# Optimization experiments

Measured on AMD Instinct MI355X. Metric: run time of the kernel, lower is better.

The kernel has to match this reference:

```python
import jax, jax.numpy as jnp
import numpy as np

N_NODES = 50000
N_EDGES = 800000
IN_DIM, HID_DIM, LAT_DIM = 64, 64, 32


def _glorot(key, fan_in, fan_out):
    s = jnp.sqrt(6.0 / (fan_in + fan_out))
    return jax.random.uniform(key, (fan_in, fan_out), jnp.float32, -s, s)


def setup_inputs() -> dict:
    key = jax.random.key(0)
    ks = jax.random.split(key, 8)
    x = jax.random.normal(ks[0], (N_NODES, IN_DIM), jnp.float32)
    edge_index = jax.random.randint(ks[1], (2, N_EDGES), 0, N_NODES, jnp.int64)
    W1 = _glorot(ks[2], IN_DIM, HID_DIM)
    b1 = jnp.zeros((HID_DIM,), jnp.float32)
    W2 = _glorot(ks[3], HID_DIM, HID_DIM)
    b2 = jnp.zeros((HID_DIM,), jnp.float32)
    W3 = _glorot(ks[4], HID_DIM, LAT_DIM)
    b3 = jnp.zeros((LAT_DIM,), jnp.float32)
    return {"x": x, "edge_index": edge_index, "W1": W1, "b1": b1,
            "W2": W2, "b2": b2, "W3": W3, "b3": b3}


def _self_loop_edges(edge_index, n):
    loop = jnp.arange(n, dtype=edge_index.dtype)
    src = jnp.concatenate([edge_index[0], loop])
    dst = jnp.concatenate([edge_index[1], loop])
    return src, dst


def _gcn_norm(src, dst, n):
    # deg over A + I (unit edge weights), computed on target column (PyG default)
    deg = jax.ops.segment_sum(jnp.ones_like(dst, dtype=jnp.float32), dst, num_segments=n)
    dinv = jnp.where(deg > 0, jax.lax.rsqrt(deg), 0.0)
    return dinv[src] * dinv[dst]  # [E+N]


def _gcn_conv(x, src, dst, norm, W, b, n):
    h = x @ W                         # [N, out] small GEMM first, as in PyG
    msg = h[src] * norm[:, None]      # gather + scale, [E+N, out]
    out = jax.ops.segment_sum(msg, dst, num_segments=n)  # scatter-add
    return out + b


def reference(x, edge_index, W1, b1, W2, b2, W3, b3):
    n = x.shape[0]
    src, dst = _self_loop_edges(edge_index, n)
    norm = _gcn_norm(src, dst, n)
    h = jnp.tanh(_gcn_conv(x, src, dst, norm, W1, b1, n))
    h = jnp.tanh(_gcn_conv(h, src, dst, norm, W2, b2, n))
    z = _gcn_conv(h, src, dst, norm, W3, b3, n)
    return z
```

## Files before the change

### kernel.cpp

```cpp
#include <hip/hip_runtime.h>
#include <hip/hip_fp16.h>
#include <type_traits>


#define IN_DIM 64
#define HID_DIM 64
#define LAT_DIM 32
#define BCAP 5120

typedef __attribute__((ext_vector_type(8))) _Float16 half8;
typedef __attribute__((ext_vector_type(4))) _Float16 half4;


__global__ __launch_bounds__(256) void bin_kernel(const int* __restrict__ src,
                                                  const int* __restrict__ dst,
                                                  int* __restrict__ bucket_cnt,
                                                  unsigned* __restrict__ pairs, int E) {
    __shared__ int bcnt[256];
    __shared__ int bbase[256];
    int tid = threadIdx.x;
    bcnt[tid] = 0;
    __syncthreads();
    int base = blockIdx.x * 4096;
    unsigned pk[16]; int bk[16]; int rk[16];
    #pragma unroll
    for (int i = 0; i < 16; ++i) {
        int e = base + i * 256 + tid;
        bk[i] = -1;
        if (e < E) {
            int s = __builtin_nontemporal_load(src + e);
            int d = __builtin_nontemporal_load(dst + e);
            bk[i] = d >> 8;
            pk[i] = (unsigned)s | ((unsigned)(d & 255) << 16);
            rk[i] = atomicAdd(&bcnt[bk[i]], 1);
        }
    }
    __syncthreads();
    int c = bcnt[tid];
    if (c > 0) bbase[tid] = atomicAdd(&bucket_cnt[tid], c);
    __syncthreads();
    #pragma unroll
    for (int i = 0; i < 16; ++i) {
        if (bk[i] >= 0) {
            int pos = bbase[bk[i]] + rk[i];
            if (pos < BCAP) pairs[(size_t)bk[i] * BCAP + pos] = pk[i];
        }
    }
}

__global__ __launch_bounds__(256) void build_csr_kernel(const unsigned* __restrict__ pairs,
                                                        const int* __restrict__ bucket_cnt,
                                                        int* __restrict__ off,
                                                        float* __restrict__ dinv,
                                                        int* __restrict__ col,
                                                        int N, int NBK) {
    __shared__ int sboff[256];
    __shared__ int h[256];
    __shared__ int scur[256];
    __shared__ int wtot[4];
    int b = blockIdx.x, tid = threadIdx.x;
    int lane = tid & 63, wid = tid >> 6;

    int v = (tid < NBK) ? min(bucket_cnt[tid], BCAP) : 0;
    int sc = v;
    #pragma unroll
    for (int d = 1; d < 64; d <<= 1) {
        int t = __shfl_up(sc, d, 64);
        if (lane >= d) sc += t;
    }
    if (lane == 63) wtot[wid] = sc;
    h[tid] = 0;
    __syncthreads();
    int woff = 0;
    #pragma unroll
    for (int w = 0; w < 4; ++w) if (w < wid) woff += wtot[w];
    sboff[tid] = woff + sc - v;
    __syncthreads();
    int boff_b = sboff[b];

    int c = min(bucket_cnt[b], BCAP);
    const unsigned* pb = pairs + (size_t)b * BCAP;
    for (int i = tid; i < c; i += 256)
        atomicAdd(&h[pb[i] >> 16], 1);
    __syncthreads();

    int hv = h[tid];
    int sc2 = hv;
    #pragma unroll
    for (int d = 1; d < 64; d <<= 1) {
        int t = __shfl_up(sc2, d, 64);
        if (lane >= d) sc2 += t;
    }
    if (lane == 63) wtot[wid] = sc2;
    __syncthreads();
    int woff2 = 0;
    #pragma unroll
    for (int w = 0; w < 4; ++w) if (w < wid) woff2 += wtot[w];
    int incl = woff2 + sc2;
    int node = b * 256 + tid;
    scur[tid] = boff_b + incl - hv;
    if (node < N) {
        off[node + 1] = boff_b + incl;
        dinv[node]    = rsqrtf((float)(hv + 1));
    }
    if (b == 0 && tid == 0) off[0] = 0;
    __syncthreads();

    for (int i = tid; i < c; i += 256) {
        unsigned p = pb[i];
        int pos = atomicAdd(&scur[p >> 16], 1);
        col[pos] = (int)(p & 0xFFFFu);
    }
}


template<int OUT, int RT, typename TIN>
__global__ __launch_bounds__(256) void gemm_tile_kernel(const TIN* __restrict__ X,
                                                        const float* __restrict__ W,
                                                        const float* __restrict__ dinv,
                                                        _Float16* __restrict__ G, int N) {
    constexpr int CG = OUT / 4;
    static_assert(256 / CG * 4 == RT, "RT must match 4*(256/CG)");
    __shared__ float Ws[64 * OUT];
    __shared__ float Xs[RT][64 + 4];
    int tid = threadIdx.x;
    int row0 = blockIdx.x * RT;

    for (int f = 4 * tid; f < 64 * OUT; f += 1024)
        *(float4*)&Ws[f] = *(const float4*)&W[f];

    if constexpr (std::is_same<TIN, float>::value) {
        for (int f = 4 * tid; f < RT * 64; f += 1024) {
            int r = f >> 6, k0 = f & 63, gr = row0 + r;
            float4 v = (gr < N) ? *(const float4*)&X[(size_t)gr * 64 + k0]
                                : make_float4(0.f, 0.f, 0.f, 0.f);
            *(float4*)&Xs[r][k0] = v;
        }
    } else {
        for (int f = 8 * tid; f < RT * 64; f += 2048) {
            int r = f >> 6, k0 = f & 63, gr = row0 + r;
            if (gr < N) {
                half8 v = *(const half8*)&X[(size_t)gr * 64 + k0];
                #pragma unroll
                for (int i = 0; i < 8; ++i) Xs[r][k0 + i] = (float)v[i];
            } else {
                #pragma unroll
                for (int i = 0; i < 8; ++i) Xs[r][k0 + i] = 0.f;
            }
        }
    }
    __syncthreads();

    int cr = tid % CG;
    int rr = tid / CG;
    float acc[4][4] = {};
    #pragma unroll 4
    for (int k = 0; k < 64; ++k) {
        float4 bv = *(float4*)&Ws[k * OUT + 4 * cr];
        float av[4] = {Xs[4 * rr + 0][k], Xs[4 * rr + 1][k],
                       Xs[4 * rr + 2][k], Xs[4 * rr + 3][k]};
        float bb[4] = {bv.x, bv.y, bv.z, bv.w};
        #pragma unroll
        for (int j = 0; j < 4; ++j)
            #pragma unroll
            for (int i = 0; i < 4; ++i)
                acc[j][i] += av[j] * bb[i];
    }

    #pragma unroll
    for (int j = 0; j < 4; ++j) {
        int gr = row0 + 4 * rr + j;
        if (gr < N) {
            float s = dinv[gr];
            half4 o;
            #pragma unroll
            for (int i = 0; i < 4; ++i) o[i] = (_Float16)(acc[j][i] * s);
            *(half4*)&G[(size_t)gr * OUT + 4 * cr] = o;
        }
    }
}


template<int D, bool TANH, typename TOUT>
__global__ __launch_bounds__(256) void agg_kernel(const _Float16* __restrict__ G,
                           const int* __restrict__ off,
                           const int* __restrict__ col, const float* __restrict__ dinv,
                           const float* __restrict__ b, TOUT* __restrict__ H, int N) {
    constexpr int CHUNKS = D / 8;
    constexpr int EPI = 64 / CHUNKS;
    int tid  = threadIdx.x;
    int lane = tid & 63;
    int w    = tid >> 6;
    int node = blockIdx.x * 4 + w;
    if (node >= N) return;
    int grp = lane / CHUNKS;
    int c4  = lane % CHUNKS;
    int p0  = off[node];
    int total = off[node + 1] - p0 + 1;
    float acc[8] = {};
    #pragma unroll 2
    for (int base = 0; base < total; base += EPI) {
        int e = base + grp;
        if (e < total) {
            int s = (e == 0) ? node : col[p0 + e - 1];
            half8 u = *(const half8*)&G[(size_t)s * D + 8 * c4];
            #pragma unroll
            for (int i = 0; i < 8; ++i) acc[i] += (float)u[i];
        }
    }
    #pragma unroll
    for (int m = CHUNKS; m < 64; m <<= 1) {
        #pragma unroll
        for (int i = 0; i < 8; ++i) acc[i] += __shfl_xor(acc[i], m, 64);
    }
    if (grp == 0) {
        float s = dinv[node];
        float o[8];
        #pragma unroll
        for (int i = 0; i < 8; ++i) {
            o[i] = s * acc[i] + b[8 * c4 + i];
            if (TANH) o[i] = tanhf(o[i]);
        }
        if constexpr (std::is_same<TOUT, _Float16>::value) {
            half8 hv;
            #pragma unroll
            for (int i = 0; i < 8; ++i) hv[i] = (_Float16)o[i];
            *(half8*)&H[(size_t)node * D + 8 * c4] = hv;
        } else {
            float4 f0 = make_float4(o[0], o[1], o[2], o[3]);
            float4 f1 = make_float4(o[4], o[5], o[6], o[7]);
            *(float4*)&H[(size_t)node * D + 8 * c4 + 0] = f0;
            *(float4*)&H[(size_t)node * D + 8 * c4 + 4] = f1;
        }
    }
}


static inline size_t align256(size_t x) { return (x + 255) & ~(size_t)255; }

extern "C" void kernel_launch(void* const* d_in, const int* in_sizes, int n_in,
                              void* d_out, int out_size, void* d_ws, size_t ws_size,
                              hipStream_t stream) {
    const float* x   = (const float*)d_in[0];
    const int*   ei  = (const int*)d_in[1];
    const float* W1  = (const float*)d_in[2];
    const float* b1  = (const float*)d_in[3];
    const float* W2  = (const float*)d_in[4];
    const float* b2  = (const float*)d_in[5];
    const float* W3  = (const float*)d_in[6];
    const float* b3  = (const float*)d_in[7];
    float* out = (float*)d_out;

    const int N = in_sizes[0] / IN_DIM;
    const int E = in_sizes[1] / 2;
    const int* src = ei;
    const int* dst = ei + E;
    const int NBK  = (N + 255) / 256;
    const int BINB = (E + 4095) / 4096;

    char* ws = (char*)d_ws;
    size_t o = 0;
    int*       bkcnt = (int*)(ws + o);       o = align256(o + 256 * 4);
    int*       off   = (int*)(ws + o);       o = align256(o + (size_t)(N + 1) * 4);
    float*     dinv  = (float*)(ws + o);     o = align256(o + (size_t)N * 4);
    unsigned*  pairs = (unsigned*)(ws + o);  o = align256(o + (size_t)NBK * BCAP * 4);
    int*       col   = (int*)(ws + o);       o = align256(o + (size_t)E * 4);
    _Float16*  bufG  = (_Float16*)(ws + o);  o = align256(o + (size_t)N * HID_DIM * 2);
    _Float16*  bufH  = (_Float16*)(ws + o);  o = align256(o + (size_t)N * HID_DIM * 2);
    (void)ws_size;

    hipMemsetAsync(bkcnt, 0, 256 * 4, stream);
    bin_kernel<<<BINB, 256, 0, stream>>>(src, dst, bkcnt, pairs, E);
    build_csr_kernel<<<NBK, 256, 0, stream>>>(pairs, bkcnt, off, dinv, col, N, NBK);

    const int g64_grid = (N + 63) / 64;
    const int g32_grid = (N + 127) / 128;
    const int agg_grid = (N + 3) / 4;

    gemm_tile_kernel<HID_DIM, 64, float><<<g64_grid, 256, 0, stream>>>(x, W1, dinv, bufG, N);
    agg_kernel<HID_DIM, true, _Float16><<<agg_grid, 256, 0, stream>>>(bufG, off, col, dinv, b1, bufH, N);
    gemm_tile_kernel<HID_DIM, 64, _Float16><<<g64_grid, 256, 0, stream>>>(bufH, W2, dinv, bufG, N);
    agg_kernel<HID_DIM, true, _Float16><<<agg_grid, 256, 0, stream>>>(bufG, off, col, dinv, b2, bufH, N);
    gemm_tile_kernel<LAT_DIM, 128, _Float16><<<g32_grid, 256, 0, stream>>>(bufH, W3, dinv, bufG, N);
    agg_kernel<LAT_DIM, false, float><<<agg_grid, 256, 0, stream>>>(bufG, off, col, dinv, b3, out, N);
}
```

Measured before the change: 236.3 us.

## Fuse aggregation with next layer's dense transform into persistent kernel

Aggregation for layers 1 and 2 now applies tanh and then multiplies by the next weight matrix inside the same wave, using shuffles and a weight tile held in shared memory. This replaces two separate GEMM kernels and removes the write and re-read of the intermediate hidden activations. The fused kernel uses a grid-stride persistent loop with 2048 blocks. The per-node 64x64 matvec through shuffles adds ALU and LDS work, and the last aggregation kernel's unroll factor is raised.

```diff
diff --git a/kernel.cpp b/kernel.cpp
--- a/kernel.cpp
+++ b/kernel.cpp
@@ -114,8 +114,8 @@
 }
 
 
-template<int OUT, int RT, typename TIN>
-__global__ __launch_bounds__(256) void gemm_tile_kernel(const TIN* __restrict__ X,
+template<int OUT, int RT>
+__global__ __launch_bounds__(256) void gemm_tile_kernel(const float* __restrict__ X,
                                                         const float* __restrict__ W,
                                                         const float* __restrict__ dinv,
                                                         _Float16* __restrict__ G, int N) {
@@ -129,25 +129,11 @@
     for (int f = 4 * tid; f < 64 * OUT; f += 1024)
         *(float4*)&Ws[f] = *(const float4*)&W[f];
 
-    if constexpr (std::is_same<TIN, float>::value) {
-        for (int f = 4 * tid; f < RT * 64; f += 1024) {
-            int r = f >> 6, k0 = f & 63, gr = row0 + r;
-            float4 v = (gr < N) ? *(const float4*)&X[(size_t)gr * 64 + k0]
-                                : make_float4(0.f, 0.f, 0.f, 0.f);
-            *(float4*)&Xs[r][k0] = v;
-        }
-    } else {
-        for (int f = 8 * tid; f < RT * 64; f += 2048) {
-            int r = f >> 6, k0 = f & 63, gr = row0 + r;
-            if (gr < N) {
-                half8 v = *(const half8*)&X[(size_t)gr * 64 + k0];
-                #pragma unroll
-                for (int i = 0; i < 8; ++i) Xs[r][k0 + i] = (float)v[i];
-            } else {
-                #pragma unroll
-                for (int i = 0; i < 8; ++i) Xs[r][k0 + i] = 0.f;
-            }
-        }
+    for (int f = 4 * tid; f < RT * 64; f += 1024) {
+        int r = f >> 6, k0 = f & 63, gr = row0 + r;
+        float4 v = (gr < N) ? *(const float4*)&X[(size_t)gr * 64 + k0]
+                            : make_float4(0.f, 0.f, 0.f, 0.f);
+        *(float4*)&Xs[r][k0] = v;
     }
     __syncthreads();
 
@@ -181,11 +167,76 @@
 }
 
 
-template<int D, bool TANH, typename TOUT>
+template<int DOUT>
+__global__ __launch_bounds__(256) void agg_gemm_kernel(const _Float16* __restrict__ G,
+                            const int* __restrict__ off, const int* __restrict__ col,
+                            const float* __restrict__ dinv, const float* __restrict__ bias,
+                            const float* __restrict__ W, _Float16* __restrict__ G2,
+                            int N) {
+    __shared__ float Ws[64 * DOUT];
+    int tid = threadIdx.x;
+    for (int f = 4 * tid; f < 64 * DOUT; f += 1024)
+        *(float4*)&Ws[f] = *(const float4*)&W[f];
+    __syncthreads();
+
+    int lane = tid & 63, w = tid >> 6;
+    int grp = lane >> 3, c4 = lane & 7;
+    int stride = gridDim.x * 4;
+
+    for (int node = blockIdx.x * 4 + w; node < N; node += stride) {
+        int p0 = off[node];
+        int total = off[node + 1] - p0 + 1;
+        float acc[8] = {};
+        #pragma unroll 4
+        for (int base = 0; base < total; base += 8) {
+            int e = base + grp;
+            if (e < total) {
+                int s = (e == 0) ? node : col[p0 + e - 1];
+                half8 u = *(const half8*)&G[(size_t)s * 64 + 8 * c4];
+                #pragma unroll
+                for (int i = 0; i < 8; ++i) acc[i] += (float)u[i];
+            }
+        }
+        #pragma unroll
+        for (int m = 8; m < 64; m <<= 1) {
+            #pragma unroll
+            for (int i = 0; i < 8; ++i) acc[i] += __shfl_xor(acc[i], m, 64);
+        }
+        float dn = dinv[node];
+        float o[8];
+        #pragma unroll
+        for (int i = 0; i < 8; ++i) o[i] = tanhf(dn * acc[i] + bias[8 * c4 + i]);
+
+        float outv = 0.f;
+        if constexpr (DOUT == 64) {
+            int c = lane;
+            #pragma unroll
+            for (int k = 0; k < 64; ++k) {
+                float hk = __shfl(o[k & 7], k >> 3, 64);
+                outv += hk * Ws[k * 64 + c];
+            }
+        } else {
+            int c = lane & 31, kh = lane >> 5;
+            #pragma unroll
+            for (int kk = 0; kk < 32; ++kk) {
+                int k = kh * 32 + kk;
+                float hk = __shfl(o[k & 7], k >> 3, 64);
+                outv += hk * Ws[k * DOUT + c];
+            }
+            outv += __shfl_xor(outv, 32, 64);
+        }
+        outv *= dn;
+        if (DOUT == 64 || lane < 32)
+            G2[(size_t)node * DOUT + (DOUT == 64 ? lane : (lane & 31))] = (_Float16)outv;
+    }
+}
+
+
+template<int D>
 __global__ __launch_bounds__(256) void agg_kernel(const _Float16* __restrict__ G,
                            const int* __restrict__ off,
                            const int* __restrict__ col, const float* __restrict__ dinv,
-                           const float* __restrict__ b, TOUT* __restrict__ H, int N) {
+                           const float* __restrict__ b, float* __restrict__ H, int N) {
     constexpr int CHUNKS = D / 8;
     constexpr int EPI = 64 / CHUNKS;
     int tid  = threadIdx.x;
@@ -198,7 +249,7 @@
     int p0  = off[node];
     int total = off[node + 1] - p0 + 1;
     float acc[8] = {};
-    #pragma unroll 2
+    #pragma unroll 4
     for (int base = 0; base < total; base += EPI) {
         int e = base + grp;
         if (e < total) {
@@ -215,23 +266,13 @@
     }
     if (grp == 0) {
         float s = dinv[node];
-        float o[8];
-        #pragma unroll
-        for (int i = 0; i < 8; ++i) {
-            o[i] = s * acc[i] + b[8 * c4 + i];
-            if (TANH) o[i] = tanhf(o[i]);
-        }
-        if constexpr (std::is_same<TOUT, _Float16>::value) {
-            half8 hv;
-            #pragma unroll
-            for (int i = 0; i < 8; ++i) hv[i] = (_Float16)o[i];
-            *(half8*)&H[(size_t)node * D + 8 * c4] = hv;
-        } else {
-            float4 f0 = make_float4(o[0], o[1], o[2], o[3]);
-            float4 f1 = make_float4(o[4], o[5], o[6], o[7]);
-            *(float4*)&H[(size_t)node * D + 8 * c4 + 0] = f0;
-            *(float4*)&H[(size_t)node * D + 8 * c4 + 4] = f1;
-        }
+        float4 f0, f1;
+        f0.x = s * acc[0] + b[8 * c4 + 0]; f0.y = s * acc[1] + b[8 * c4 + 1];
+        f0.z = s * acc[2] + b[8 * c4 + 2]; f0.w = s * acc[3] + b[8 * c4 + 3];
+        f1.x = s * acc[4] + b[8 * c4 + 4]; f1.y = s * acc[5] + b[8 * c4 + 5];
+        f1.z = s * acc[6] + b[8 * c4 + 6]; f1.w = s * acc[7] + b[8 * c4 + 7];
+        *(float4*)&H[(size_t)node * D + 8 * c4 + 0] = f0;
+        *(float4*)&H[(size_t)node * D + 8 * c4 + 4] = f1;
     }
 }
 
@@ -266,7 +307,7 @@
     unsigned*  pairs = (unsigned*)(ws + o);  o = align256(o + (size_t)NBK * BCAP * 4);
     int*       col   = (int*)(ws + o);       o = align256(o + (size_t)E * 4);
     _Float16*  bufG  = (_Float16*)(ws + o);  o = align256(o + (size_t)N * HID_DIM * 2);
-    _Float16*  bufH  = (_Float16*)(ws + o);  o = align256(o + (size_t)N * HID_DIM * 2);
+    _Float16*  bufG2 = (_Float16*)(ws + o);  o = align256(o + (size_t)N * HID_DIM * 2);
     (void)ws_size;
 
     hipMemsetAsync(bkcnt, 0, 256 * 4, stream);
@@ -274,13 +315,11 @@
     build_csr_kernel<<<NBK, 256, 0, stream>>>(pairs, bkcnt, off, dinv, col, N, NBK);
 
     const int g64_grid = (N + 63) / 64;
-    const int g32_grid = (N + 127) / 128;
     const int agg_grid = (N + 3) / 4;
-
-    gemm_tile_kernel<HID_DIM, 64, float><<<g64_grid, 256, 0, stream>>>(x, W1, dinv, bufG, N);
-    agg_kernel<HID_DIM, true, _Float16><<<agg_grid, 256, 0, stream>>>(bufG, off, col, dinv, b1, bufH, N);
-    gemm_tile_kernel<HID_DIM, 64, _Float16><<<g64_grid, 256, 0, stream>>>(bufH, W2, dinv, bufG, N);
-    agg_kernel<HID_DIM, true, _Float16><<<agg_grid, 256, 0, stream>>>(bufG, off, col, dinv, b2, bufH, N);
-    gemm_tile_kernel<LAT_DIM, 128, _Float16><<<g32_grid, 256, 0, stream>>>(bufH, W3, dinv, bufG, N);
-    agg_kernel<LAT_DIM, false, float><<<agg_grid, 256, 0, stream>>>(bufG, off, col, dinv, b3, out, N);
-}
+    const int fus_grid = 2048;
+
+    gemm_tile_kernel<HID_DIM, 64><<<g64_grid, 256, 0, stream>>>(x, W1, dinv, bufG, N);
+    agg_gemm_kernel<64><<<fus_grid, 256, 0, stream>>>(bufG, off, col, dinv, b1, W2, bufG2, N);
+    agg_gemm_kernel<32><<<fus_grid, 256, 0, stream>>>(bufG2, off, col, dinv, b2, W3, bufG, N);
+    agg_kernel<LAT_DIM><<<agg_grid, 256, 0, stream>>>(bufG, off, col, dinv, b3, out, N);
+}
```

Result: slower. 245.6 us (+3.9%).
